# Optimization experiments

Hardware: AMD Instinct MI355X
Metric: run time of the kernel (lower is better)

## Reference

```python
import jax, jax.numpy as jnp
import numpy as np

# TT-matrix dense layer: y = relu(x @ M + b) where M is a TT-matrix with cores
# G_k of shape [r_{k-1}, m_k, n_k, r_k], M[i1..id, j1..jd] = G1[:,i1,j1,:] ... Gd[:,id,jd,:]

IN_DIMS = [8, 8, 8, 8]
OUT_DIMS = [8, 8, 8, 8]
RANKS = [1, 8, 8, 8, 1]
BATCH = 4096


def setup_inputs() -> dict:
    key = jax.random.key(0)
    ks = jax.random.split(key, 6)
    inp = {"x": jax.random.normal(ks[0], (BATCH, int(np.prod(IN_DIMS))), dtype=jnp.float32)}
    # glorot-ish scale for TT cores so that the reconstructed matrix has sane variance
    for k in range(4):
        shape = (RANKS[k], IN_DIMS[k], OUT_DIMS[k], RANKS[k + 1])
        scale = 0.3
        inp[f"core{k}"] = scale * jax.random.normal(ks[1 + k], shape, dtype=jnp.float32)
    inp["b"] = 0.1 * jnp.ones((int(np.prod(OUT_DIMS)),), dtype=jnp.float32)
    return inp


def _tt_matmul(x, cores):
    # x: [B, prod(m)], cores[k]: [r_{k-1}, m_k, n_k, r_k]
    B = x.shape[0]
    ms = [G.shape[1] for G in cores]
    # res: [a, r, m_k, t] with a = B * prod(n_done), t = prod(m_rest)
    res = x.reshape(B, 1, ms[0], -1)
    for k, G in enumerate(cores):
        a, _, _, t = res.shape
        n, r_next = G.shape[2], G.shape[3]
        # contract rank and current input mode: [a, n, r_next, t]
        res = jnp.einsum('aqmt,qmnr->anrt', res, G)
        m_next = ms[k + 1] if k + 1 < len(cores) else 1
        res = res.reshape(a * n, r_next, m_next, t // m_next)
    return res.reshape(B, -1)  # [B, prod(n)], big-endian output index order


def reference(x, core0, core1, core2, core3, b):
    y = _tt_matmul(x, [core0, core1, core2, core3])
    return jax.nn.relu(y + b)
```

## Files before the change

kernel.cpp:

```cpp
#include <hip/hip_runtime.h>
#include <hip/hip_bf16.h>
#include <stdint.h>

typedef short bf16x8 __attribute__((ext_vector_type(8)));
typedef float f32x4 __attribute__((ext_vector_type(4)));
typedef unsigned short u16;
typedef u16 ushort8 __attribute__((ext_vector_type(8)));

typedef __attribute__((address_space(3))) void lds_void;
typedef const __attribute__((address_space(1))) void gbl_void;

#define BAR() do { asm volatile("" ::: "memory"); __builtin_amdgcn_s_barrier(); asm volatile("" ::: "memory"); } while (0)
#define WAITV(N) asm volatile("s_waitcnt vmcnt(" #N ")" ::: "memory")
#define LGKM0() asm volatile("s_waitcnt lgkmcnt(0)" ::: "memory")

__device__ __forceinline__ u16 f2bf(float f) {
  uint32_t u = __builtin_bit_cast(uint32_t, f);
  u += 0x7fffu + ((u >> 16) & 1u);
  return (u16)(u >> 16);
}

__global__ __launch_bounds__(256) void prep_fused(
    const float* __restrict__ x, u16* __restrict__ xb,
    const float* __restrict__ c0, const float* __restrict__ c1,
    const float* __restrict__ c2, const float* __restrict__ c3,
    u16* __restrict__ Mt) {
  const int t = threadIdx.x;
  if (blockIdx.x >= 4096) {
    const int i = ((blockIdx.x - 4096) * 256 + t) * 8;
    float4 a = *(const float4*)(x + i);
    float4 b = *(const float4*)(x + i + 4);
    ushort8 o;
    o[0] = f2bf(a.x); o[1] = f2bf(a.y); o[2] = f2bf(a.z); o[3] = f2bf(a.w);
    o[4] = f2bf(b.x); o[5] = f2bf(b.y); o[6] = f2bf(b.z); o[7] = f2bf(b.w);
    *(ushort8*)(xb + i) = o;
    return;
  }
  const int bid = blockIdx.x;
  const int j1 = bid & 7, i1 = (bid >> 3) & 7, j0 = (bid >> 6) & 7, i0 = bid >> 9;
  __shared__ float v[512];
  __shared__ float g3[512];
  g3[t] = c3[t];
  g3[t + 256] = c3[t + 256];
  float w2[8];
#pragma unroll
  for (int r2 = 0; r2 < 8; ++r2) {
    float s = 0.f;
#pragma unroll
    for (int r1 = 0; r1 < 8; ++r1)
      s += c0[(i0 * 8 + j0) * 8 + r1] * c1[((r1 * 8 + i1) * 8 + j1) * 8 + r2];
    w2[r2] = s;
  }
#pragma unroll
  for (int e = t; e < 512; e += 256) {
    const int r3 = e & 7, j2 = (e >> 3) & 7, i2 = e >> 6;
    float s = 0.f;
#pragma unroll
    for (int r2 = 0; r2 < 8; ++r2)
      s += w2[r2] * c2[((r2 * 8 + i2) * 8 + j2) * 8 + r3];
    v[e] = s;
  }
  __syncthreads();
  const int jr = t >> 2, ic0 = (t & 3) * 16;
  const int j2 = jr >> 3, j3 = jr & 7;
  const size_t base =
      (size_t)(j0 * 512 + j1 * 64 + jr) * 4096 + (i0 * 512 + i1 * 64) + ic0;
  ushort8 o0, o1;
#pragma unroll
  for (int q = 0; q < 16; ++q) {
    const int ic = ic0 + q, i2 = ic >> 3, i3 = ic & 7;
    float s = 0.f;
#pragma unroll
    for (int r3 = 0; r3 < 8; ++r3)
      s += v[(i2 << 6) + (j2 << 3) + r3] * g3[(r3 << 6) + (i3 << 3) + j3];
    const u16 h = f2bf(s);
    if (q < 8) o0[q] = h; else o1[q - 8] = h;
  }
  *(ushort8*)(Mt + base) = o0;
  *(ushort8*)(Mt + base + 8) = o1;
}

__global__ __launch_bounds__(512, 2) void gemm_bias_relu(
    const u16* __restrict__ A, const u16* __restrict__ Bt,
    const float* __restrict__ bias, float* __restrict__ C) {
  constexpr int K = 4096, N = 4096, NT = 64;
  __shared__ __align__(16) char lds[131072];
  const int t = threadIdx.x;
  const int l = t & 63, w = t >> 6;
  const int wr = w >> 2, wc = w & 3;
  const int lr = l & 15, lk = l >> 4;
  const int bm = blockIdx.y, bn = blockIdx.x;

  const char* gA = (const char*)A + (size_t)bm * 256 * (K * 2);
  const char* gB = (const char*)Bt + (size_t)bn * 256 * (K * 2);
  const int srow = t >> 3;
  const int schunk = (t & 7) ^ (srow & 7);
  const int sgo = srow * (K * 2) + schunk * 16;
  const int sld = t * 16;

  const int axor = (lk ^ (lr & 7)) * 16;
  const int aoff0 = (wr * 128 + lr) * 128 + axor;
  const int aoff1 = aoff0 ^ 64;
  const int boff0 = 65536 + (wc * 64 + lr) * 128 + axor;
  const int boff1 = boff0 ^ 64;

  auto stA = [&](int p, int h, int kt) {
    const char* src = gA + (size_t)(h * 128) * (K * 2) + kt * 128 + sgo;
    char* dst = lds + p * 32768 + h * 16384 + sld;
    __builtin_amdgcn_global_load_lds((gbl_void*)src, (lds_void*)dst, 16, 0, 0);
    __builtin_amdgcn_global_load_lds((gbl_void*)(src + (size_t)64 * (K * 2)),
                                     (lds_void*)(dst + 8192), 16, 0, 0);
  };
  auto stB = [&](int p, int h, int kt) {
    const char* src = gB + (size_t)(h * 128) * (K * 2) + kt * 128 + sgo;
    char* dst = lds + 65536 + p * 32768 + h * 16384 + sld;
    __builtin_amdgcn_global_load_lds((gbl_void*)src, (lds_void*)dst, 16, 0, 0);
    __builtin_amdgcn_global_load_lds((gbl_void*)(src + (size_t)64 * (K * 2)),
                                     (lds_void*)(dst + 8192), 16, 0, 0);
  };
  auto rdA = [&](int p, int off, int m) -> bf16x8 {
    return *(const bf16x8*)(lds + p * 32768 + off + m * 2048);
  };
  auto rdB = [&](int p, int off, int n) -> bf16x8 {
    return *(const bf16x8*)(lds + p * 32768 + off + n * 2048);
  };

  bf16x8 aH0[8], aH1[8], bH0[4], bH1[4];
  f32x4 acc[8][4];
#pragma unroll
  for (int m = 0; m < 8; ++m)
#pragma unroll
    for (int n = 0; n < 4; ++n) acc[m][n] = f32x4{0.f, 0.f, 0.f, 0.f};

  auto rdAH = [&](bf16x8* d, int p, int mh) {
#pragma unroll
    for (int m2 = 0; m2 < 4; ++m2) {
      d[m2 * 2 + 0] = rdA(p, aoff0, mh * 4 + m2);
      d[m2 * 2 + 1] = rdA(p, aoff1, mh * 4 + m2);
    }
  };
  auto rdBH = [&](bf16x8* d, int p, int nh) {
#pragma unroll
    for (int n2 = 0; n2 < 2; ++n2) {
      d[n2 * 2 + 0] = rdB(p, boff0, nh * 2 + n2);
      d[n2 * 2 + 1] = rdB(p, boff1, nh * 2 + n2);
    }
  };
  auto quad = [&](int mh, int nh, bf16x8* aH, bf16x8* bH) {
    __builtin_amdgcn_s_setprio(1);
#pragma unroll
    for (int kk = 0; kk < 2; ++kk)
#pragma unroll
      for (int m2 = 0; m2 < 4; ++m2)
#pragma unroll
        for (int n2 = 0; n2 < 2; ++n2)
          acc[mh * 4 + m2][nh * 2 + n2] = __builtin_amdgcn_mfma_f32_16x16x32_bf16(
              aH[m2 * 2 + kk], bH[n2 * 2 + kk], acc[mh * 4 + m2][nh * 2 + n2], 0, 0, 0);
    __builtin_amdgcn_s_setprio(0);
  };

  stA(0, 0, 0); stA(0, 1, 0); stB(0, 0, 0); stB(0, 1, 0);
  stB(1, 0, 1); stB(1, 1, 1);
  WAITV(4);
  BAR();
  rdAH(aH0, 0, 0); rdBH(bH0, 0, 0);
  stA(1, 0, 1);
  BAR();

  for (int it = 0; it < NT / 2; ++it) {
    const int T = 2 * it;
    const int t2 = (T + 2 < NT) ? T + 2 : NT - 1;
    const int t3 = (T + 3 < NT) ? T + 3 : NT - 1;
    rdBH(bH1, 0, 1);
    quad(0, 0, aH0, bH0);
    stA(1, 1, T + 1);
    BAR();
    rdAH(aH1, 0, 1);
    quad(0, 1, aH0, bH1);
    stB(0, 0, t2);
    BAR();
    quad(1, 1, aH1, bH1);
    stB(0, 1, t2); stA(0, 0, t2);
    WAITV(6);
    BAR();
    rdAH(aH0, 1, 0);
    quad(1, 0, aH1, bH0);
    rdBH(bH0, 1, 0);
    stA(0, 1, t2);
    BAR();
    rdBH(bH1, 1, 1);
    quad(0, 0, aH0, bH0);
    BAR();
    rdAH(aH1, 1, 1);
    quad(0, 1, aH0, bH1);
    stB(1, 0, t3);
    BAR();
    quad(1, 1, aH1, bH1);
    stB(1, 1, t3);
    WAITV(4);
    BAR();
    rdAH(aH0, 0, 0);
    quad(1, 0, aH1, bH0);
    rdBH(bH0, 0, 0);
    stA(1, 0, t3);
    BAR();
  }
  WAITV(0);

  const int row0 = bm * 256 + wr * 128;
  const int col0 = bn * 256 + wc * 64;
#pragma unroll
  for (int n = 0; n < 4; ++n) {
    const int col = col0 + n * 16 + lr;
    const float bv = bias[col];
#pragma unroll
    for (int m = 0; m < 8; ++m) {
      const int r0 = row0 + m * 16 + lk * 4;
#pragma unroll
      for (int vv = 0; vv < 4; ++vv) {
        const float val = acc[m][n][vv] + bv;
        C[(size_t)(r0 + vv) * N + col] = val > 0.f ? val : 0.f;
      }
    }
  }
}

extern "C" void kernel_launch(void* const* d_in, const int* in_sizes, int n_in,
                              void* d_out, int out_size, void* d_ws, size_t ws_size,
                              hipStream_t stream) {
  const float* x  = (const float*)d_in[0];
  const float* c0 = (const float*)d_in[1];
  const float* c1 = (const float*)d_in[2];
  const float* c2 = (const float*)d_in[3];
  const float* c3 = (const float*)d_in[4];
  const float* b  = (const float*)d_in[5];
  float* out = (float*)d_out;

  u16* xb  = (u16*)d_ws;
  u16* mtb = xb + (size_t)4096 * 4096;

  prep_fused<<<dim3(4096 + 8192), dim3(256), 0, stream>>>(x, xb, c0, c1, c2, c3, mtb);
  gemm_bias_relu<<<dim3(16, 16), dim3(512), 0, stream>>>(xb, mtb, b, out);
}
```

Baseline: 135.3 us.

## Switch GEMM inner loop from 16x16x32 to 32x32x16 bf16 MFMA tiles

Replaces the 16x16x32 MFMA tiling with 32x32x16 MFMA instructions, reorganizing per-wave operand fragments (4 M-blocks x 2 N-blocks of 32x32) and the quad schedule so that each quad covers a K-half and an N-block rather than an M/N quadrant. The LDS read addressing and swizzle are recomputed for the 32-lane row layout, and the epilogue is rewritten for the 32x32 accumulator layout. Larger MFMA tiles reduce the number of matrix instructions and the operand reloads per FLOP, but they change register pressure and LDS bank access patterns, and the epilogue now writes 16 rows per lane with strided row indices.

```diff
diff --git a/kernel.cpp b/kernel.cpp
--- a/kernel.cpp
+++ b/kernel.cpp
@@ -3,7 +3,7 @@
 #include <stdint.h>
 
 typedef short bf16x8 __attribute__((ext_vector_type(8)));
-typedef float f32x4 __attribute__((ext_vector_type(4)));
+typedef float f32x16 __attribute__((ext_vector_type(16)));
 typedef unsigned short u16;
 typedef u16 ushort8 __attribute__((ext_vector_type(8)));
 
@@ -12,7 +12,6 @@
 
 #define BAR() do { asm volatile("" ::: "memory"); __builtin_amdgcn_s_barrier(); asm volatile("" ::: "memory"); } while (0)
 #define WAITV(N) asm volatile("s_waitcnt vmcnt(" #N ")" ::: "memory")
-#define LGKM0() asm volatile("s_waitcnt lgkmcnt(0)" ::: "memory")
 
 __device__ __forceinline__ u16 f2bf(float f) {
   uint32_t u = __builtin_bit_cast(uint32_t, f);
@@ -88,7 +87,7 @@
   const int t = threadIdx.x;
   const int l = t & 63, w = t >> 6;
   const int wr = w >> 2, wc = w & 3;
-  const int lr = l & 15, lk = l >> 4;
+  const int l31 = l & 31;
   const int bm = blockIdx.y, bn = blockIdx.x;
 
   const char* gA = (const char*)A + (size_t)bm * 256 * (K * 2);
@@ -98,11 +97,9 @@
   const int sgo = srow * (K * 2) + schunk * 16;
   const int sld = t * 16;
 
-  const int axor = (lk ^ (lr & 7)) * 16;
-  const int aoff0 = (wr * 128 + lr) * 128 + axor;
-  const int aoff1 = aoff0 ^ 64;
-  const int boff0 = 65536 + (wc * 64 + lr) * 128 + axor;
-  const int boff1 = boff0 ^ 64;
+  const int cbase = ((l >> 5) ^ (l & 7)) * 16;
+  const int aoff00 = (wr * 128 + l31) * 128 + cbase;
+  const int boff00 = 65536 + (wc * 64 + l31) * 128 + cbase;
 
   auto stA = [&](int p, int h, int kt) {
     const char* src = gA + (size_t)(h * 128) * (K * 2) + kt * 128 + sgo;
@@ -118,44 +115,40 @@
     __builtin_amdgcn_global_load_lds((gbl_void*)(src + (size_t)64 * (K * 2)),
                                      (lds_void*)(dst + 8192), 16, 0, 0);
   };
-  auto rdA = [&](int p, int off, int m) -> bf16x8 {
-    return *(const bf16x8*)(lds + p * 32768 + off + m * 2048);
-  };
-  auto rdB = [&](int p, int off, int n) -> bf16x8 {
-    return *(const bf16x8*)(lds + p * 32768 + off + n * 2048);
-  };
 
   bf16x8 aH0[8], aH1[8], bH0[4], bH1[4];
-  f32x4 acc[8][4];
-#pragma unroll
-  for (int m = 0; m < 8; ++m)
-#pragma unroll
-    for (int n = 0; n < 4; ++n) acc[m][n] = f32x4{0.f, 0.f, 0.f, 0.f};
-
-  auto rdAH = [&](bf16x8* d, int p, int mh) {
-#pragma unroll
-    for (int m2 = 0; m2 < 4; ++m2) {
-      d[m2 * 2 + 0] = rdA(p, aoff0, mh * 4 + m2);
-      d[m2 * 2 + 1] = rdA(p, aoff1, mh * 4 + m2);
-    }
-  };
-  auto rdBH = [&](bf16x8* d, int p, int nh) {
-#pragma unroll
-    for (int n2 = 0; n2 < 2; ++n2) {
-      d[n2 * 2 + 0] = rdB(p, boff0, nh * 2 + n2);
-      d[n2 * 2 + 1] = rdB(p, boff1, nh * 2 + n2);
-    }
-  };
-  auto quad = [&](int mh, int nh, bf16x8* aH, bf16x8* bH) {
+  f32x16 acc[4][2];
+#pragma unroll
+  for (int mb = 0; mb < 4; ++mb)
+#pragma unroll
+    for (int nb = 0; nb < 2; ++nb)
+#pragma unroll
+      for (int r = 0; r < 16; ++r) acc[mb][nb][r] = 0.f;
+
+  auto rdAH = [&](bf16x8* d, int p, int kh) {
+#pragma unroll
+    for (int mb = 0; mb < 4; ++mb)
+#pragma unroll
+      for (int ks = 0; ks < 2; ++ks)
+        d[mb * 2 + ks] = *(const bf16x8*)(lds + p * 32768 +
+            ((aoff00 + mb * 4096) ^ (ks * 32) ^ (kh * 64)));
+  };
+  auto rdBH = [&](bf16x8* d, int p, int nb) {
+#pragma unroll
+    for (int kh = 0; kh < 2; ++kh)
+#pragma unroll
+      for (int ks = 0; ks < 2; ++ks)
+        d[kh * 2 + ks] = *(const bf16x8*)(lds + p * 32768 +
+            ((boff00 + nb * 4096) ^ (ks * 32) ^ (kh * 64)));
+  };
+  auto quad = [&](int kh, int nb, bf16x8* aH, bf16x8* bH) {
     __builtin_amdgcn_s_setprio(1);
 #pragma unroll
-    for (int kk = 0; kk < 2; ++kk)
-#pragma unroll
-      for (int m2 = 0; m2 < 4; ++m2)
-#pragma unroll
-        for (int n2 = 0; n2 < 2; ++n2)
-          acc[mh * 4 + m2][nh * 2 + n2] = __builtin_amdgcn_mfma_f32_16x16x32_bf16(
-              aH[m2 * 2 + kk], bH[n2 * 2 + kk], acc[mh * 4 + m2][nh * 2 + n2], 0, 0, 0);
+    for (int ks = 0; ks < 2; ++ks)
+#pragma unroll
+      for (int mb = 0; mb < 4; ++mb)
+        acc[mb][nb] = __builtin_amdgcn_mfma_f32_32x32x16_bf16(
+            aH[mb * 2 + ks], bH[kh * 2 + ks], acc[mb][nb], 0, 0, 0);
     __builtin_amdgcn_s_setprio(0);
   };
 
@@ -209,17 +202,18 @@
 
   const int row0 = bm * 256 + wr * 128;
   const int col0 = bn * 256 + wc * 64;
-#pragma unroll
-  for (int n = 0; n < 4; ++n) {
-    const int col = col0 + n * 16 + lr;
+  const int rsub = 4 * (l >> 5);
+#pragma unroll
+  for (int nb = 0; nb < 2; ++nb) {
+    const int col = col0 + nb * 32 + l31;
     const float bv = bias[col];
 #pragma unroll
-    for (int m = 0; m < 8; ++m) {
-      const int r0 = row0 + m * 16 + lk * 4;
-#pragma unroll
-      for (int vv = 0; vv < 4; ++vv) {
-        const float val = acc[m][n][vv] + bv;
-        C[(size_t)(r0 + vv) * N + col] = val > 0.f ? val : 0.f;
+    for (int mb = 0; mb < 4; ++mb) {
+#pragma unroll
+      for (int r = 0; r < 16; ++r) {
+        const int row = row0 + mb * 32 + (r & 3) + 8 * (r >> 2) + rsub;
+        const float val = acc[mb][nb][r] + bv;
+        C[(size_t)row * N + col] = val > 0.f ? val : 0.f;
       }
     }
   }
```

Measured after the change: 150.2 us. 1.11x slower.
